# Optimization experiments

Hardware: AMD Instinct MI355X
Metric: run time of the kernel (lower is better)

## Reference

```python
import jax, jax.numpy as jnp
import numpy as np

DIM = 384
NUM_HEADS = 12
WIN = (8, 8, 8)
Q_TOK = 1
K_TOK = 1
B = 64
N = WIN[0] * WIN[1] * WIN[2]  # 512


def _build_rel_index():
    t = max(Q_TOK, K_TOK)
    max_rel = [(w - 1) * t for w in WIN]
    nbins = [2 * m + 1 for m in max_rel]
    def coords(tok):
        axes = [np.arange(WIN[i]) * tok for i in range(3)]
        g = np.stack(np.meshgrid(*axes, indexing='ij'))  # [3, D, H, W]
        return g.reshape(3, -1)  # [3, N]
    cq = coords(Q_TOK)
    ck = coords(K_TOK)
    rel = (cq[:, :, None] - ck[:, None, :]).transpose(1, 2, 0)  # [N, N, 3]
    rel = rel + np.array(max_rel)
    idx = rel[..., 0] * (nbins[1] * nbins[2]) + rel[..., 1] * nbins[2] + rel[..., 2]
    return idx.astype(np.int32), nbins[0] * nbins[1] * nbins[2]


def setup_inputs() -> dict:
    key = jax.random.key(0)
    ks = jax.random.split(key, 7)
    rel_index_np, num_rel = _build_rel_index()
    s = 0.02
    return {
        'x1': jax.random.normal(ks[0], (B, N, DIM), jnp.float32),
        'x2': jax.random.normal(ks[1], (B, N, DIM), jnp.float32),
        'Wq': jax.random.normal(ks[2], (DIM, DIM), jnp.float32) * s,
        'Wkv': jax.random.normal(ks[3], (2 * DIM, DIM), jnp.float32) * s,
        'q_bias': jax.random.normal(ks[4], (DIM,), jnp.float32) * s,
        'v_bias': jax.random.normal(ks[5], (DIM,), jnp.float32) * s,
        'bias_table': jax.random.normal(ks[6], (num_rel, NUM_HEADS), jnp.float32) * s,
        'rel_index': jnp.asarray(rel_index_np),  # [N, N] int32
    }


def reference(x1, x2, Wq, Wkv, q_bias, v_bias, bias_table, rel_index):
    Bq, N1, C = x1.shape
    N2 = x2.shape[1]
    H = NUM_HEADS
    hd = C // H

    q = x1 @ Wq.T + q_bias                      # [B, N1, C]
    kv_bias = jnp.concatenate([jnp.zeros_like(v_bias), v_bias])
    kv = x2 @ Wkv.T + kv_bias                   # [B, N2, 2C]

    q = q.reshape(Bq, N1, H, hd).transpose(0, 2, 1, 3)   # [B, H, N1, hd]
    kv = kv.reshape(Bq, N2, 2, H, hd).transpose(2, 0, 3, 1, 4)
    k, v = kv[0], kv[1]                          # [B, H, N2, hd]

    # relative position bias: gather [N1, N2, H] -> [H, N1, N2]
    bias = bias_table[rel_index]                 # [N1, N2, H]
    bias = bias.transpose(2, 0, 1)               # [H, N1, N2]

    scale = 1.0 / jnp.sqrt(jnp.asarray(hd, q.dtype))
    scores = jnp.einsum('bhqd,bhkd->bhqk', q, k) * scale + bias[None]
    attn = jax.nn.softmax(scores, axis=-1)
    out = jnp.einsum('bhqk,bhkd->bhqd', attn, v)  # [B, H, N1, hd]
    return out.transpose(0, 2, 1, 3).reshape(Bq, N1, C)
```

## Files before the change

kernel.cpp:

```cpp
#include <hip/hip_runtime.h>

typedef unsigned short u16;
typedef unsigned int u32;
typedef __bf16 bf16x8 __attribute__((ext_vector_type(8)));
typedef float f32x4 __attribute__((ext_vector_type(4)));
typedef u16 u16x4 __attribute__((ext_vector_type(4)));
typedef u16 u16x8 __attribute__((ext_vector_type(8)));
typedef u32 u32x4 __attribute__((ext_vector_type(4)));

#define NB 64
#define NN 512
#define NH 12
#define HD 32
#define DIM 384

static constexpr size_t QWS = (size_t)NB * NH * NN * HD;
#define LOG2E 1.4426950408889634f
#define QSCALE 0.25503486f

__device__ __forceinline__ u16 f2bf(float f) {
  __bf16 b = (__bf16)f;
  union { __bf16 b; u16 u; } v; v.b = b;
  return v.u;
}
__device__ __forceinline__ float lo16f(u32 w) {
  union { u32 u; float f; } v; v.u = w << 16;
  return v.f;
}
__device__ __forceinline__ float hi16f(u32 w) {
  union { u32 u; float f; } v; v.u = w & 0xffff0000u;
  return v.f;
}
__device__ __forceinline__ void gload16(const void* g, void* l) {
  __builtin_amdgcn_global_load_lds((const __attribute__((address_space(1))) u32*)g,
                                   (__attribute__((address_space(3))) u32*)l, 16, 0, 0);
}

__global__ __launch_bounds__(256) void prep_k(const float* __restrict__ table,
                                              const int* __restrict__ rel,
                                              const float* __restrict__ Wq,
                                              const float* __restrict__ Wkv,
                                              u32* __restrict__ beR,
                                              u16* __restrict__ Wf) {
  int bid = blockIdx.x;
  if (bid < 6144) {
    int t = bid * 256 + threadIdx.x;
    int word = t & 3;
    int lane = (t >> 2) & 63;
    int mf   = (t >> 8) & 3;
    int wv   = (t >> 10) & 7;
    int kt   = (t >> 13) & 15;
    int h    = t >> 17;
    int lr = lane & 15, lg = lane >> 4;
    int q = wv * 64 + mf * 16 + lr;
    int k = kt * 32 + (word >> 1) * 16 + lg * 4 + (word & 1) * 2;
    int i0 = rel[q * NN + k];
    int i1 = rel[q * NN + k + 1];
    u16 b0 = f2bf(table[i0 * NH + h] * LOG2E);
    u16 b1 = f2bf(table[i1 * NH + h] * LOG2E);
    beR[t] = (u32)b0 | ((u32)b1 << 16);
  } else {
    int t2 = (bid - 6144) * 256 + threadIdx.x;
    int lane = t2 & 63;
    int kk = (t2 >> 6) % 12;
    int cb = t2 / (12 * 64);
    int j = cb * 16 + (lane & 15);
    int k = kk * 32 + (lane >> 4) * 8;
    const float* wrow = (j < 384) ? (Wq + (size_t)j * DIM) : (Wkv + (size_t)(j - 384) * DIM);
    float4 a = *(const float4*)(wrow + k);
    float4 b = *(const float4*)(wrow + k + 4);
    u16x8 o = {f2bf(a.x), f2bf(a.y), f2bf(a.z), f2bf(a.w),
               f2bf(b.x), f2bf(b.y), f2bf(b.z), f2bf(b.w)};
    *(u16x8*)(Wf + (size_t)t2 * 8) = o;
  }
}

__global__ __launch_bounds__(256, 3) void qkv_proj_k(const float* __restrict__ x1,
                                                     const float* __restrict__ x2,
                                                     const float* __restrict__ qb,
                                                     const float* __restrict__ vb,
                                                     const u16* __restrict__ Wf,
                                                     u16* __restrict__ q_ws,
                                                     u16* __restrict__ k_ws,
                                                     u16* __restrict__ v_ws) {
  __shared__ __attribute__((aligned(16))) u16 Wbuf[2][12288];

  const int g = blockIdx.x;
  const int vv = (g & 7) * 96 + (g >> 3);
  const int type = vv >> 8;
  const int m0 = (vv & 255) * 128;
  const int tid = threadIdx.x, lane = tid & 63, w = tid >> 6;
  const int lg = lane >> 4, lr = lane & 15;
  const float* X = (type == 0) ? x1 : x2;
  const int bb = m0 >> 9, m0r = m0 & 511;
  const char* wsrc = (const char*)(Wf + (size_t)type * 24 * 6144);

  bf16x8 aflo[12], afhi[12];
  {
    const float* xlo = X + (size_t)(m0 + w * 32 + lr) * DIM + lg * 8;
    const float* xhi = xlo + (size_t)16 * DIM;
#pragma unroll
    for (int kk = 0; kk < 12; ++kk) {
      float4 a = *(const float4*)(xlo + kk * 32);
      float4 b = *(const float4*)(xlo + kk * 32 + 4);
      aflo[kk] = (bf16x8){(__bf16)a.x, (__bf16)a.y, (__bf16)a.z, (__bf16)a.w,
                          (__bf16)b.x, (__bf16)b.y, (__bf16)b.z, (__bf16)b.w};
      float4 c = *(const float4*)(xhi + kk * 32);
      float4 d = *(const float4*)(xhi + kk * 32 + 4);
      afhi[kk] = (bf16x8){(__bf16)c.x, (__bf16)c.y, (__bf16)c.z, (__bf16)c.w,
                          (__bf16)d.x, (__bf16)d.y, (__bf16)d.z, (__bf16)d.w};
    }
  }

#pragma unroll
  for (int i = 0; i < 6; ++i) {
    int off = (i * 256 + tid) * 16;
    gload16(wsrc + off, (char*)&Wbuf[0][0] + off);
  }
  __syncthreads();

  u16* dst = (type == 0) ? q_ws : (type == 1 ? k_ws : v_ws);
  const float* bias = (type == 0) ? qb : (type == 2 ? vb : nullptr);
  const float scale = (type == 0) ? QSCALE : 1.0f;

  for (int c = 0; c < 12; ++c) {
    if (c + 1 < 12) {
      const char* s = wsrc + (size_t)(c + 1) * 24576;
      char* d = (char*)&Wbuf[(c + 1) & 1][0];
#pragma unroll
      for (int i = 0; i < 6; ++i) {
        int off = (i * 256 + tid) * 16;
        gload16(s + off, d + off);
      }
    }
    const u16* wb = &Wbuf[c & 1][0];
    f32x4 acc[2][2] = {};
#pragma unroll
    for (int kk = 0; kk < 12; ++kk) {
      bf16x8 wf0 = *(const bf16x8*)(wb + (kk * 64 + lane) * 8);
      bf16x8 wf1 = *(const bf16x8*)(wb + ((12 + kk) * 64 + lane) * 8);
      acc[0][0] = __builtin_amdgcn_mfma_f32_16x16x32_bf16(wf0, aflo[kk], acc[0][0], 0, 0, 0);
      acc[0][1] = __builtin_amdgcn_mfma_f32_16x16x32_bf16(wf0, afhi[kk], acc[0][1], 0, 0, 0);
      acc[1][0] = __builtin_amdgcn_mfma_f32_16x16x32_bf16(wf1, aflo[kk], acc[1][0], 0, 0, 0);
      acc[1][1] = __builtin_amdgcn_mfma_f32_16x16x32_bf16(wf1, afhi[kk], acc[1][1], 0, 0, 0);
    }
#pragma unroll
    for (int lc = 0; lc < 2; ++lc) {
      int cb = c * 2 + lc;
      int head = cb >> 1;
      int d0 = (cb & 1) * 16 + lg * 4;
      float4 bv = {0.f, 0.f, 0.f, 0.f};
      if (type != 1) bv = *(const float4*)(bias + head * 32 + d0);
#pragma unroll
      for (int rg = 0; rg < 2; ++rg) {
        int n = m0r + w * 32 + rg * 16 + lr;
        u16x4 o = {f2bf((acc[lc][rg][0] + bv.x) * scale),
                   f2bf((acc[lc][rg][1] + bv.y) * scale),
                   f2bf((acc[lc][rg][2] + bv.z) * scale),
                   f2bf((acc[lc][rg][3] + bv.w) * scale)};
        *(u16x4*)(dst + ((size_t)(bb * NH + head) * NN + n) * HD + d0) = o;
      }
    }
    __syncthreads();
  }
}

__global__ __launch_bounds__(512, 4) void attn_k(const u16* __restrict__ qw,
                                                 const u16* __restrict__ kw,
                                                 const u16* __restrict__ vw,
                                                 const u32* __restrict__ beR,
                                                 float* __restrict__ out) {
  const int g = blockIdx.x;
  const int vv = (g & 7) * 96 + (g >> 3);
  const int h = vv >> 6, b = vv & 63;
  const size_t base = ((size_t)b * NH + h) * NN * HD;
  const u16* Q = qw + base;
  const u16* K = kw + base;
  const u16* V = vw + base;

  __shared__ u16 Ks[NN][40];
  __shared__ u16 Vtp[HD][520];

  const int tid = threadIdx.x;
  const int lane = tid & 63, w = tid >> 6;
  const int lg = lane >> 4, lr = lane & 15;
  const int q0 = w * 64;

  bf16x8 qf[4];
#pragma unroll
  for (int mf = 0; mf < 4; ++mf)
    qf[mf] = *(const bf16x8*)&Q[(q0 + mf * 16 + lr) * HD + lg * 8];

  for (int c = tid; c < 2048; c += 512) {
    int row = c >> 2, part = (c & 3) * 8;
    *(u16x8*)&Ks[row][part] = *(const u16x8*)&K[row * HD + part];
    u16x8 vld = *(const u16x8*)&V[row * HD + part];
    int kk = row & 31;
    int col = (row & ~31) + ((kk >> 2) & 3) * 8 + (kk >> 4) * 4 + (kk & 3);
#pragma unroll
    for (int j = 0; j < 8; ++j) Vtp[part + j][col] = vld[j];
  }
  __syncthreads();

  const u32* bstream = beR + ((((size_t)h * 16) * 8 + w) * 4) * 256 + lane * 4;

  f32x4 accOT[4][2] = {};
  float lsum[4] = {0.f, 0.f, 0.f, 0.f};

  for (int kt = 0; kt < 16; ++kt) {
    const int k0 = kt * 32;
    const u32* bkt = bstream + (size_t)kt * 8192;
    bf16x8 kf0 = *(const bf16x8*)&Ks[k0 + lr][lg * 8];
    bf16x8 kf1 = *(const bf16x8*)&Ks[k0 + 16 + lr][lg * 8];
    bf16x8 vp0 = *(const bf16x8*)&Vtp[lr][k0 + lg * 8];
    bf16x8 vp1 = *(const bf16x8*)&Vtp[16 + lr][k0 + lg * 8];
#pragma unroll
    for (int mf = 0; mf < 4; ++mf) {
      u32x4 bbv = *(const u32x4*)(bkt + mf * 256);
      f32x4 c0 = {lo16f(bbv.x), hi16f(bbv.x), lo16f(bbv.y), hi16f(bbv.y)};
      f32x4 c1 = {lo16f(bbv.z), hi16f(bbv.z), lo16f(bbv.w), hi16f(bbv.w)};
      f32x4 s0 = __builtin_amdgcn_mfma_f32_16x16x32_bf16(kf0, qf[mf], c0, 0, 0, 0);
      f32x4 s1 = __builtin_amdgcn_mfma_f32_16x16x32_bf16(kf1, qf[mf], c1, 0, 0, 0);
      float p0[4], p1[4];
#pragma unroll
      for (int r = 0; r < 4; ++r) {
        p0[r] = __builtin_amdgcn_exp2f(s0[r]);
        p1[r] = __builtin_amdgcn_exp2f(s1[r]);
      }
      lsum[mf] += ((p0[0] + p0[1]) + (p0[2] + p0[3])) +
                  ((p1[0] + p1[1]) + (p1[2] + p1[3]));
      bf16x8 pv = {(__bf16)p0[0], (__bf16)p0[1], (__bf16)p0[2], (__bf16)p0[3],
                   (__bf16)p1[0], (__bf16)p1[1], (__bf16)p1[2], (__bf16)p1[3]};
      accOT[mf][0] = __builtin_amdgcn_mfma_f32_16x16x32_bf16(vp0, pv, accOT[mf][0], 0, 0, 0);
      accOT[mf][1] = __builtin_amdgcn_mfma_f32_16x16x32_bf16(vp1, pv, accOT[mf][1], 0, 0, 0);
    }
  }

  float linv[4];
#pragma unroll
  for (int mf = 0; mf < 4; ++mf) {
    float s = lsum[mf];
    s += __shfl_xor(s, 16, 64);
    s += __shfl_xor(s, 32, 64);
    linv[mf] = 1.0f / s;
  }

  float* outp = out + ((size_t)b * NN) * DIM + h * HD;
#pragma unroll
  for (int mf = 0; mf < 4; ++mf) {
    int q = q0 + mf * 16 + lr;
#pragma unroll
    for (int nf = 0; nf < 2; ++nf) {
      float4 o = {accOT[mf][nf][0] * linv[mf], accOT[mf][nf][1] * linv[mf],
                  accOT[mf][nf][2] * linv[mf], accOT[mf][nf][3] * linv[mf]};
      *(float4*)&outp[(size_t)q * DIM + nf * 16 + lg * 4] = o;
    }
  }
}

extern "C" void kernel_launch(void* const* d_in, const int* in_sizes, int n_in,
                              void* d_out, int out_size, void* d_ws, size_t ws_size,
                              hipStream_t stream) {
  const float* x1    = (const float*)d_in[0];
  const float* x2    = (const float*)d_in[1];
  const float* Wq    = (const float*)d_in[2];
  const float* Wkv   = (const float*)d_in[3];
  const float* qb    = (const float*)d_in[4];
  const float* vb    = (const float*)d_in[5];
  const float* table = (const float*)d_in[6];
  const int*   rel   = (const int*)d_in[7];
  float* out = (float*)d_out;

  u16* ws   = (u16*)d_ws;
  u16* q_ws = ws;
  u16* k_ws = ws + QWS;
  u16* v_ws = ws + 2 * QWS;
  u32* beR  = (u32*)(ws + 3 * QWS);
  u16* Wf   = ws + 3 * QWS + 2 * 1572864;

  prep_k<<<6360, 256, 0, stream>>>(table, rel, Wq, Wkv, beR, Wf);
  qkv_proj_k<<<768, 256, 0, stream>>>(x1, x2, qb, vb, Wf, q_ws, k_ws, v_ws);
  attn_k<<<NB * NH, 512, 0, stream>>>(q_ws, k_ws, v_ws, beR, out);
}
```

Before: 111.7 us.

## Restructure QKV projection: per-wave weight columns from global, 32-row blocks

The QKV projection kernel drops the double-buffered LDS weight staging and its barriers. Each block now handles 32 rows instead of 128, and each wave loads its own 6 column blocks of pre-swizzled weights straight from global/L2 into registers. The grid grows from 768 to 3072 blocks. This removes LDS traffic and synchronisation and raises parallelism. In exchange, every block redundantly reads a quarter of the weight matrix from global memory, and each wave's weight loads are no longer overlapped with compute.

Result: slower. 200.5 us (+79.5%).

```diff
diff --git a/kernel.cpp b/kernel.cpp
--- a/kernel.cpp
+++ b/kernel.cpp
@@ -30,10 +30,6 @@
 __device__ __forceinline__ float hi16f(u32 w) {
   union { u32 u; float f; } v; v.u = w & 0xffff0000u;
   return v.f;
-}
-__device__ __forceinline__ void gload16(const void* g, void* l) {
-  __builtin_amdgcn_global_load_lds((const __attribute__((address_space(1))) u32*)g,
-                                   (__attribute__((address_space(3))) u32*)l, 16, 0, 0);
 }
 
 __global__ __launch_bounds__(256) void prep_k(const float* __restrict__ table,
@@ -83,85 +79,61 @@
                                                      u16* __restrict__ q_ws,
                                                      u16* __restrict__ k_ws,
                                                      u16* __restrict__ v_ws) {
-  __shared__ __attribute__((aligned(16))) u16 Wbuf[2][12288];
-
   const int g = blockIdx.x;
-  const int vv = (g & 7) * 96 + (g >> 3);
-  const int type = vv >> 8;
-  const int m0 = (vv & 255) * 128;
+  const int vv = (g & 7) * 384 + (g >> 3);
+  const int type = vv >> 10;
+  const int m0 = (vv & 1023) * 32;
   const int tid = threadIdx.x, lane = tid & 63, w = tid >> 6;
   const int lg = lane >> 4, lr = lane & 15;
   const float* X = (type == 0) ? x1 : x2;
   const int bb = m0 >> 9, m0r = m0 & 511;
-  const char* wsrc = (const char*)(Wf + (size_t)type * 24 * 6144);
-
-  bf16x8 aflo[12], afhi[12];
+
+  bf16x8 af0[12], af1[12];
   {
-    const float* xlo = X + (size_t)(m0 + w * 32 + lr) * DIM + lg * 8;
+    const float* xlo = X + (size_t)(m0 + lr) * DIM + lg * 8;
     const float* xhi = xlo + (size_t)16 * DIM;
 #pragma unroll
     for (int kk = 0; kk < 12; ++kk) {
       float4 a = *(const float4*)(xlo + kk * 32);
       float4 b = *(const float4*)(xlo + kk * 32 + 4);
-      aflo[kk] = (bf16x8){(__bf16)a.x, (__bf16)a.y, (__bf16)a.z, (__bf16)a.w,
-                          (__bf16)b.x, (__bf16)b.y, (__bf16)b.z, (__bf16)b.w};
+      af0[kk] = (bf16x8){(__bf16)a.x, (__bf16)a.y, (__bf16)a.z, (__bf16)a.w,
+                         (__bf16)b.x, (__bf16)b.y, (__bf16)b.z, (__bf16)b.w};
       float4 c = *(const float4*)(xhi + kk * 32);
       float4 d = *(const float4*)(xhi + kk * 32 + 4);
-      afhi[kk] = (bf16x8){(__bf16)c.x, (__bf16)c.y, (__bf16)c.z, (__bf16)c.w,
-                          (__bf16)d.x, (__bf16)d.y, (__bf16)d.z, (__bf16)d.w};
-    }
-  }
-
-#pragma unroll
-  for (int i = 0; i < 6; ++i) {
-    int off = (i * 256 + tid) * 16;
-    gload16(wsrc + off, (char*)&Wbuf[0][0] + off);
-  }
-  __syncthreads();
+      af1[kk] = (bf16x8){(__bf16)c.x, (__bf16)c.y, (__bf16)c.z, (__bf16)c.w,
+                         (__bf16)d.x, (__bf16)d.y, (__bf16)d.z, (__bf16)d.w};
+    }
+  }
 
   u16* dst = (type == 0) ? q_ws : (type == 1 ? k_ws : v_ws);
   const float* bias = (type == 0) ? qb : (type == 2 ? vb : nullptr);
   const float scale = (type == 0) ? QSCALE : 1.0f;
 
-  for (int c = 0; c < 12; ++c) {
-    if (c + 1 < 12) {
-      const char* s = wsrc + (size_t)(c + 1) * 24576;
-      char* d = (char*)&Wbuf[(c + 1) & 1][0];
-#pragma unroll
-      for (int i = 0; i < 6; ++i) {
-        int off = (i * 256 + tid) * 16;
-        gload16(s + off, d + off);
-      }
-    }
-    const u16* wb = &Wbuf[c & 1][0];
-    f32x4 acc[2][2] = {};
+  for (int cw = 0; cw < 6; ++cw) {
+    int cb = w * 6 + cw;
+    const u16* wc = Wf + (((size_t)(type * 24 + cb) * 12) * 64 + lane) * 8;
+    bf16x8 wf[12];
+#pragma unroll
+    for (int kk = 0; kk < 12; ++kk)
+      wf[kk] = *(const bf16x8*)(wc + (size_t)kk * 512);
+    f32x4 a0 = {0.f, 0.f, 0.f, 0.f};
+    f32x4 a1 = {0.f, 0.f, 0.f, 0.f};
 #pragma unroll
     for (int kk = 0; kk < 12; ++kk) {
-      bf16x8 wf0 = *(const bf16x8*)(wb + (kk * 64 + lane) * 8);
-      bf16x8 wf1 = *(const bf16x8*)(wb + ((12 + kk) * 64 + lane) * 8);
-      acc[0][0] = __builtin_amdgcn_mfma_f32_16x16x32_bf16(wf0, aflo[kk], acc[0][0], 0, 0, 0);
-      acc[0][1] = __builtin_amdgcn_mfma_f32_16x16x32_bf16(wf0, afhi[kk], acc[0][1], 0, 0, 0);
-      acc[1][0] = __builtin_amdgcn_mfma_f32_16x16x32_bf16(wf1, aflo[kk], acc[1][0], 0, 0, 0);
-      acc[1][1] = __builtin_amdgcn_mfma_f32_16x16x32_bf16(wf1, afhi[kk], acc[1][1], 0, 0, 0);
-    }
-#pragma unroll
-    for (int lc = 0; lc < 2; ++lc) {
-      int cb = c * 2 + lc;
-      int head = cb >> 1;
-      int d0 = (cb & 1) * 16 + lg * 4;
-      float4 bv = {0.f, 0.f, 0.f, 0.f};
-      if (type != 1) bv = *(const float4*)(bias + head * 32 + d0);
-#pragma unroll
-      for (int rg = 0; rg < 2; ++rg) {
-        int n = m0r + w * 32 + rg * 16 + lr;
-        u16x4 o = {f2bf((acc[lc][rg][0] + bv.x) * scale),
-                   f2bf((acc[lc][rg][1] + bv.y) * scale),
-                   f2bf((acc[lc][rg][2] + bv.z) * scale),
-                   f2bf((acc[lc][rg][3] + bv.w) * scale)};
-        *(u16x4*)(dst + ((size_t)(bb * NH + head) * NN + n) * HD + d0) = o;
-      }
-    }
-    __syncthreads();
+      a0 = __builtin_amdgcn_mfma_f32_16x16x32_bf16(wf[kk], af0[kk], a0, 0, 0, 0);
+      a1 = __builtin_amdgcn_mfma_f32_16x16x32_bf16(wf[kk], af1[kk], a1, 0, 0, 0);
+    }
+    int head = cb >> 1;
+    int d0 = (cb & 1) * 16 + lg * 4;
+    float4 bv = {0.f, 0.f, 0.f, 0.f};
+    if (type != 1) bv = *(const float4*)(bias + head * 32 + d0);
+    size_t obase = ((size_t)(bb * NH + head) * NN + m0r + lr) * HD + d0;
+    u16x4 o0 = {f2bf((a0[0] + bv.x) * scale), f2bf((a0[1] + bv.y) * scale),
+                f2bf((a0[2] + bv.z) * scale), f2bf((a0[3] + bv.w) * scale)};
+    *(u16x4*)(dst + obase) = o0;
+    u16x4 o1 = {f2bf((a1[0] + bv.x) * scale), f2bf((a1[1] + bv.y) * scale),
+                f2bf((a1[2] + bv.z) * scale), f2bf((a1[3] + bv.w) * scale)};
+    *(u16x4*)(dst + obase + (size_t)16 * HD) = o1;
   }
 }
 
@@ -279,6 +251,6 @@
   u16* Wf   = ws + 3 * QWS + 2 * 1572864;
 
   prep_k<<<6360, 256, 0, stream>>>(table, rel, Wq, Wkv, beR, Wf);
-  qkv_proj_k<<<768, 256, 0, stream>>>(x1, x2, qb, vb, Wf, q_ws, k_ws, v_ws);
+  qkv_proj_k<<<3072, 256, 0, stream>>>(x1, x2, qb, vb, Wf, q_ws, k_ws, v_ws);
   attn_k<<<NB * NH, 512, 0, stream>>>(q_ws, k_ws, v_ws, beR, out);
 }
```
